# Optimization experiments

Hardware: AMD Instinct MI355X
Metric: run time of the kernel (lower is better)

The kernel has to match this reference:

```python
import jax, jax.numpy as jnp
import numpy as np

N_NODES = 50000
N_PAIRS = 200000
HID1 = 256
HID2 = 32


def gcn_conv(x, src, dst, W, b, n):
    # PyG GCNConv: project, add self-loops, sym-normalize, scatter-add to dst.
    sl = jnp.arange(n, dtype=src.dtype)
    s = jnp.concatenate([src, sl])
    d = jnp.concatenate([dst, sl])
    deg = jnp.zeros((n,), x.dtype).at[d].add(1.0)
    dinv = jax.lax.rsqrt(deg)  # deg >= 1 due to self-loops
    xw = x @ W  # [n, out]
    msg = xw[s] * (dinv[s] * dinv[d])[:, None]  # [E+n, out]
    out = jax.ops.segment_sum(msg, d, num_segments=n)
    return out + b


def setup_inputs() -> dict:
    key = jax.random.key(0)
    ks = jax.random.split(key, 16)
    inp = {
        "x": jax.random.randint(ks[0], (N_NODES,), 0, N_NODES),
        "edge1": jax.random.randint(ks[1], (2, 1600000), 0, N_NODES),
        "pos": jax.random.randint(ks[2], (N_PAIRS, 2), 0, N_NODES),
        "idx": jax.random.randint(ks[3], (N_PAIRS,), 0, N_PAIRS),
        "ei2": jax.random.randint(ks[4], (2, 1600000), 0, N_PAIRS),
        "emb_table": jax.random.normal(ks[5], (N_NODES + 1, HID1), jnp.float32) * 0.02,
        "W1": jax.random.normal(ks[6], (HID1, HID2), jnp.float32) * (1.0 / np.sqrt(HID1)),
        "b1": jnp.zeros((HID2,), jnp.float32),
        "W2a": jax.random.normal(ks[7], (HID2, HID2), jnp.float32) * (1.0 / np.sqrt(HID2)),
        "b2a": jnp.zeros((HID2,), jnp.float32),
        "W2b": jax.random.normal(ks[8], (HID2, HID2), jnp.float32) * (1.0 / np.sqrt(HID2)),
        "b2b": jnp.zeros((HID2,), jnp.float32),
        "Wp": jax.random.normal(ks[9], (HID2, 1), jnp.float32) * (1.0 / np.sqrt(HID2)),
        "bp": jnp.zeros((1,), jnp.float32),
    }
    return inp


def reference(x, edge1, pos, idx, ei2, emb_table, W1, b1, W2a, b2a, W2b, b2b, Wp, bp):
    # eval mode: all Dropouts are identity; no LayerNorm/GraphNorm (default flags False)
    h = emb_table[x]  # [N, HID1] embedding lookup (squeeze is no-op for 1D ids)
    # conv1s: single GCNConv HID1 -> HID2 + ReLU
    h = jax.nn.relu(gcn_conv(h, edge1[0], edge1[1], W1, b1, N_NODES))
    # pairwise gather-multiply over pos
    h = h[pos[:, 0]] * h[pos[:, 1]]  # [M, HID2]
    # conv2s / conv2s_r on the pair graph (edge2 = ei2, edge2_r = flipped)
    h = (jax.nn.relu(gcn_conv(h, ei2[0], ei2[1], W2a, b2a, N_PAIRS))
         + jax.nn.relu(gcn_conv(h, ei2[1], ei2[0], W2b, b2b, N_PAIRS)))
    # gather by idx, then multiply consecutive (even, odd) rows
    h = h[idx]  # [2Q, HID2]
    h = h[0::2] * h[1::2]  # [Q, HID2]
    return h @ Wp + bp  # [Q, 1]
```

## Files before the change

kernel.cpp:

```cpp
#include <hip/hip_runtime.h>
#include <hip/hip_fp16.h>
#include <math.h>


#define SL     256
#define SLOG   8
#define SL1    64
#define SLOG1  6
#define CAP    2432
#define SHIFT  18
#define BCH    8192
#define BT     1024
#define EPT    8
#define MAXSL2 1024
#define PB     64
#define EROW   264

typedef short bf16x8 __attribute__((ext_vector_type(8)));
typedef float f32x4 __attribute__((ext_vector_type(4)));

static __device__ __forceinline__ unsigned short f2bf(float f) {
    union { float f; unsigned u; } v;
    v.f = f;
    unsigned r = v.u + 0x7FFF + ((v.u >> 16) & 1);
    return (unsigned short)(r >> 16);
}
static __device__ __forceinline__ float bf2f(unsigned short h) {
    return __uint_as_float(((unsigned)h) << 16);
}
static __device__ __forceinline__ float bflo(unsigned u) { return __uint_as_float(u << 16); }
static __device__ __forceinline__ float bfhi(unsigned u) { return __uint_as_float(u & 0xFFFF0000u); }

static __device__ __forceinline__ float4 bfacc(float4 a, uint2 w) {
    a.x += bflo(w.x);
    a.y += bfhi(w.x);
    a.z += bflo(w.y);
    a.w += bfhi(w.y);
    return a;
}
static __device__ __forceinline__ float4 hacc(float4 a, uint2 w) {
    float2 f0 = __half22float2(*(__half2*)&w.x);
    float2 f1 = __half22float2(*(__half2*)&w.y);
    a.x += f0.x;
    a.y += f0.y;
    a.z += f1.x;
    a.w += f1.y;
    return a;
}
static __device__ __forceinline__ float4 h2f4(uint2 w) {
    float2 f0 = __half22float2(*(__half2*)&w.x);
    float2 f1 = __half22float2(*(__half2*)&w.y);
    float4 r = {f0.x, f0.y, f1.x, f1.y};
    return r;
}
static __device__ __forceinline__ uint2 f42h(float4 f) {
    __half2 h0 = __floats2half2_rn(f.x, f.y);
    __half2 h1 = __floats2half2_rn(f.z, f.w);
    uint2 r = {*(unsigned*)&h0, *(unsigned*)&h1};
    return r;
}

__global__ __launch_bounds__(256) void k_init(int* __restrict__ bumpF,
                                              int* __restrict__ bumpR,
                                              int* __restrict__ bump1,
                                              int NS2, int NS1) {
    int i = blockIdx.x * 256 + threadIdx.x;
    if (i < NS2) {
        bumpF[i] = i * CAP;
        bumpR[i] = i * CAP;
    }
    if (i < NS1) bump1[i] = i * CAP;
}

__global__ __launch_bounds__(BT) void k_build(const int* __restrict__ s2,
                                              const int* __restrict__ d2,
                                              const int* __restrict__ s1,
                                              const int* __restrict__ d1,
                                              int* bumpF, int* bumpR, int* bump1,
                                              int* __restrict__ bktF,
                                              int* __restrict__ bktR,
                                              int* __restrict__ bkt1,
                                              const float* __restrict__ W1,
                                              const float* __restrict__ W2a,
                                              const float* __restrict__ W2b,
                                              unsigned short* __restrict__ Wbhi,
                                              unsigned short* __restrict__ Wblo,
                                              unsigned short* __restrict__ W2ah,
                                              unsigned short* __restrict__ W2al,
                                              unsigned short* __restrict__ W2bh,
                                              unsigned short* __restrict__ W2bl,
                                              int E2, int E1, int NS2, int NS1,
                                              int NB2, int NB1) {
    __shared__ int stag[BCH];
    __shared__ unsigned short stag2[BCH];
    __shared__ int lbF[MAXSL2];
    __shared__ int lbR[MAXSL2];
    __shared__ int bgF[MAXSL2], bgR[MAXSL2];
    __shared__ int wsum[BT / 64];
    int tid = threadIdx.x, bid = blockIdx.x;
    int lane = tid & 63, wid = tid >> 6;

    auto exscan = [&](int v) -> int {
        int sc = v;
#pragma unroll
        for (int d = 1; d < 64; d <<= 1) {
            int t = __shfl_up(sc, d, 64);
            if (lane >= d) sc += t;
        }
        if (lane == 63) wsum[wid] = sc;
        __syncthreads();
        int woff = 0;
        for (int w2 = 0; w2 < wid; w2++) woff += wsum[w2];
        __syncthreads();
        return woff + sc - v;
    };

    if (bid < NB2) {
        if (tid < NS2) { lbF[tid] = 0; lbR[tid] = 0; }
        __syncthreads();
        int eb = bid * BCH;
        int n = E2 - eb; if (n > BCH) n = BCH;
        int sv[EPT], dv[EPT], ofF[EPT], ofR[EPT];
#pragma unroll
        for (int k = 0; k < EPT; k++) {
            int i = k * BT + tid;
            if (i < n) {
                sv[k] = s2[eb + i];
                dv[k] = d2[eb + i];
                ofF[k] = atomicAdd(&lbF[dv[k] >> SLOG], 1);
                ofR[k] = atomicAdd(&lbR[sv[k] >> SLOG], 1);
            }
        }
        __syncthreads();
        int cF = (tid < NS2) ? lbF[tid] : 0;
        int cR = (tid < NS2) ? lbR[tid] : 0;
        int preF = exscan(cF);
        int preR = exscan(cR);
        if (tid < NS2) {
            lbF[tid] = preF;
            lbR[tid] = preR;
            bgF[tid] = cF ? atomicAdd(&bumpF[tid], cF) : 0;
            bgR[tid] = cR ? atomicAdd(&bumpR[tid], cR) : 0;
        }
        __syncthreads();
#pragma unroll
        for (int k = 0; k < EPT; k++) {
            int i = k * BT + tid;
            if (i < n) {
                int sf = dv[k] >> SLOG;
                int p = lbF[sf] + ofF[k];
                stag[p] = ((dv[k] & (SL - 1)) << SHIFT) | sv[k];
                stag2[p] = (unsigned short)sf;
            }
        }
        __syncthreads();
        for (int i = tid; i < n; i += BT) {
            int sf = stag2[i];
            int gp = bgF[sf] + (i - lbF[sf]);
            if (gp < (sf + 1) * CAP) bktF[gp] = stag[i];
        }
        __syncthreads();
#pragma unroll
        for (int k = 0; k < EPT; k++) {
            int i = k * BT + tid;
            if (i < n) {
                int sr = sv[k] >> SLOG;
                int p = lbR[sr] + ofR[k];
                stag[p] = ((sv[k] & (SL - 1)) << SHIFT) | dv[k];
                stag2[p] = (unsigned short)sr;
            }
        }
        __syncthreads();
        for (int i = tid; i < n; i += BT) {
            int sr = stag2[i];
            int gp = bgR[sr] + (i - lbR[sr]);
            if (gp < (sr + 1) * CAP) bktR[gp] = stag[i];
        }
    } else if (bid < NB2 + NB1) {
        if (tid < NS1) lbF[tid] = 0;
        __syncthreads();
        int eb = (bid - NB2) * BCH;
        int n = E1 - eb; if (n > BCH) n = BCH;
        int sv[EPT], dv[EPT], of[EPT];
#pragma unroll
        for (int k = 0; k < EPT; k++) {
            int i = k * BT + tid;
            if (i < n) {
                sv[k] = s1[eb + i];
                dv[k] = d1[eb + i];
                of[k] = atomicAdd(&lbF[dv[k] >> SLOG1], 1);
            }
        }
        __syncthreads();
        int c = (tid < NS1) ? lbF[tid] : 0;
        int pre = exscan(c);
        if (tid < NS1) {
            lbF[tid] = pre;
            bgF[tid] = c ? atomicAdd(&bump1[tid], c) : 0;
        }
        __syncthreads();
#pragma unroll
        for (int k = 0; k < EPT; k++) {
            int i = k * BT + tid;
            if (i < n) {
                int sf = dv[k] >> SLOG1;
                int p = lbF[sf] + of[k];
                stag[p] = ((dv[k] & (SL1 - 1)) << SHIFT) | sv[k];
                stag2[p] = (unsigned short)sf;
            }
        }
        __syncthreads();
        for (int i = tid; i < n; i += BT) {
            int sf = stag2[i];
            int gp = bgF[sf] + (i - lbF[sf]);
            if (gp < (sf + 1) * CAP) bkt1[gp] = stag[i];
        }
    } else {
        int i = (bid - NB2 - NB1) * BT + tid;
        if (i < 8192) {
            int k = i >> 5, c = i & 31;
            float w = W1[i];
            unsigned short hi = f2bf(w);
            unsigned short lo = f2bf(w - bf2f(hi));
            Wbhi[c * 256 + k] = hi;
            Wblo[c * 256 + k] = lo;
        }
        if (i < 1024) {
            int k = i >> 5, c = i & 31;
            float wa = W2a[i], wb = W2b[i];
            unsigned short ha = f2bf(wa);
            unsigned short hb = f2bf(wb);
            W2ah[c * 32 + k] = ha;
            W2al[c * 32 + k] = f2bf(wa - bf2f(ha));
            W2bh[c * 32 + k] = hb;
            W2bl[c * 32 + k] = f2bf(wb - bf2f(hb));
        }
    }
}

__global__ __launch_bounds__(256) void k_sort(int* __restrict__ bkt1, const int* __restrict__ bump1,
                                              float* __restrict__ dinv1, int* __restrict__ beg1,
                                              int* __restrict__ cnt1,
                                              int* __restrict__ bktF, const int* __restrict__ bumpF,
                                              float* __restrict__ dinvF, int* __restrict__ begF,
                                              int* __restrict__ cntF,
                                              int* __restrict__ bktR, const int* __restrict__ bumpR,
                                              float* __restrict__ dinvR, int* __restrict__ begR,
                                              int* __restrict__ cntR,
                                              int NS1, int NS2, int N1, int NP) {
    __shared__ int sorted[CAP];
    __shared__ int hist[SL], cursor[SL];
    __shared__ int wsum[4];
    int bid = blockIdx.x, tid = threadIdx.x;
    int s, sls, N;
    int* bkt;
    const int* bump;
    float* dinv;
    int* beg;
    int* cntA;
    if (bid < NS1) {
        s = bid;
        bkt = bkt1; bump = bump1; dinv = dinv1; beg = beg1; cntA = cnt1;
        sls = SL1; N = N1;
    } else if (bid < NS1 + NS2) {
        s = bid - NS1;
        bkt = bktF; bump = bumpF; dinv = dinvF; beg = begF; cntA = cntF;
        sls = SL; N = NP;
    } else {
        s = bid - NS1 - NS2;
        bkt = bktR; bump = bumpR; dinv = dinvR; beg = begR; cntA = cntR;
        sls = SL; N = NP;
    }
    hist[tid] = 0;
    __syncthreads();
    int cnt = bump[s] - s * CAP;
    if (cnt > CAP) cnt = CAP;
    int* b = bkt + (size_t)s * CAP;
    for (int i = tid; i < cnt; i += 256) atomicAdd(&hist[b[i] >> SHIFT], 1);
    __syncthreads();
    int c = (tid < sls) ? hist[tid] : 0;
    int sc = c;
    int lane = tid & 63, wid = tid >> 6;
#pragma unroll
    for (int d = 1; d < 64; d <<= 1) {
        int t = __shfl_up(sc, d, 64);
        if (lane >= d) sc += t;
    }
    if (lane == 63) wsum[wid] = sc;
    __syncthreads();
    int woff = 0;
    for (int w = 0; w < wid; w++) woff += wsum[w];
    int pre = woff + sc - c;
    cursor[tid] = pre;
    if (tid < sls) {
        int v = s * sls + tid;
        if (v < N) {
            dinv[v] = 1.f / sqrtf((float)c + 1.f);
            beg[v] = s * CAP + pre;
            cntA[v] = c;
        }
    }
    __syncthreads();
    for (int i = tid; i < cnt; i += 256) {
        int pair = b[i];
        int dl = pair >> SHIFT;
        int p = atomicAdd(&cursor[dl], 1);
        sorted[p] = pair & ((1 << SHIFT) - 1);
    }
    __syncthreads();
    for (int i = tid; i < cnt; i += 256) b[i] = sorted[i];
}

__global__ __launch_bounds__(256) void k_xw1(const int* __restrict__ x,
                                             const float* __restrict__ emb,
                                             const unsigned short* __restrict__ Wbhi,
                                             const unsigned short* __restrict__ Wblo,
                                             const float* __restrict__ dinv1,
                                             __half* __restrict__ y1, int N) {
    __shared__ unsigned short sEhi[32 * EROW];
    __shared__ unsigned short sElo[32 * EROW];
    int tid = threadIdx.x;
    int lane = tid & 63, wv = tid >> 6;
    int r0 = blockIdx.x * 32;
    const float4* emb4 = (const float4*)emb;
#pragma unroll
    for (int p = 0; p < 8; p++) {
        int row = p * 4 + wv;
        int r = r0 + row;
        int xr = x[(r < N) ? r : 0];
        float4 e = emb4[(size_t)xr * 64 + lane];
        unsigned short h0 = f2bf(e.x), h1 = f2bf(e.y), h2 = f2bf(e.z), h3 = f2bf(e.w);
        ushort4 hi = {h0, h1, h2, h3};
        ushort4 lo = {f2bf(e.x - bf2f(h0)), f2bf(e.y - bf2f(h1)),
                      f2bf(e.z - bf2f(h2)), f2bf(e.w - bf2f(h3))};
        *(ushort4*)&sEhi[row * EROW + lane * 4] = hi;
        *(ushort4*)&sElo[row * EROW + lane * 4] = lo;
    }
    __syncthreads();
    int col = lane & 15, quad = lane >> 4;
    int rowtile = wv >> 1, ntile = wv & 1;
    f32x4 acc = {0.f, 0.f, 0.f, 0.f};
    const unsigned short* arow_hi = &sEhi[(rowtile * 16 + col) * EROW + quad * 8];
    const unsigned short* arow_lo = &sElo[(rowtile * 16 + col) * EROW + quad * 8];
    const unsigned short* bh = Wbhi + (ntile * 16 + col) * 256 + quad * 8;
    const unsigned short* bl = Wblo + (ntile * 16 + col) * 256 + quad * 8;
#pragma unroll
    for (int kb = 0; kb < 256; kb += 32) {
        bf16x8 ahi = *(const bf16x8*)(arow_hi + kb);
        bf16x8 alo = *(const bf16x8*)(arow_lo + kb);
        bf16x8 bhv = *(const bf16x8*)(bh + kb);
        bf16x8 blv = *(const bf16x8*)(bl + kb);
        acc = __builtin_amdgcn_mfma_f32_16x16x32_bf16(ahi, bhv, acc, 0, 0, 0);
        acc = __builtin_amdgcn_mfma_f32_16x16x32_bf16(alo, bhv, acc, 0, 0, 0);
        acc = __builtin_amdgcn_mfma_f32_16x16x32_bf16(ahi, blv, acc, 0, 0, 0);
    }
#pragma unroll
    for (int reg = 0; reg < 4; reg++) {
        int grow = r0 + rowtile * 16 + quad * 4 + reg;
        if (grow < N) {
            float dv = dinv1[grow];
            y1[grow * 32 + ntile * 16 + col] = __float2half(acc[reg] * dv);
        }
    }
}

static __device__ __forceinline__ float4 gcn_sum_h(const int* __restrict__ adj, int bg, int end,
                                                   const uint2* __restrict__ y2, int q,
                                                   float4 acc) {
    float4 a1 = {0.f, 0.f, 0.f, 0.f};
    int i = bg;
    for (; i + 4 <= end; i += 4) {
        int u0 = adj[i], u1 = adj[i + 1], u2 = adj[i + 2], u3 = adj[i + 3];
        uint2 w0 = y2[u0 * 8 + q];
        uint2 w1 = y2[u1 * 8 + q];
        uint2 w2 = y2[u2 * 8 + q];
        uint2 w3 = y2[u3 * 8 + q];
        acc = hacc(acc, w0);
        a1 = hacc(a1, w1);
        acc = hacc(acc, w2);
        a1 = hacc(a1, w3);
    }
    for (; i < end; i++) acc = hacc(acc, y2[adj[i] * 8 + q]);
    acc.x += a1.x;
    acc.y += a1.y;
    acc.z += a1.z;
    acc.w += a1.w;
    return acc;
}

static __device__ __forceinline__ float4 gcn_sum_bf(const int* __restrict__ adj, int bg, int end,
                                                    const uint2* __restrict__ y2, int q,
                                                    float4 acc) {
    float4 a1 = {0.f, 0.f, 0.f, 0.f};
    int i = bg;
    for (; i + 4 <= end; i += 4) {
        int u0 = adj[i], u1 = adj[i + 1], u2 = adj[i + 2], u3 = adj[i + 3];
        uint2 w0 = y2[u0 * 8 + q];
        uint2 w1 = y2[u1 * 8 + q];
        uint2 w2 = y2[u2 * 8 + q];
        uint2 w3 = y2[u3 * 8 + q];
        acc = bfacc(acc, w0);
        a1 = bfacc(a1, w1);
        acc = bfacc(acc, w2);
        a1 = bfacc(a1, w3);
    }
    for (; i < end; i++) acc = bfacc(acc, y2[adj[i] * 8 + q]);
    acc.x += a1.x;
    acc.y += a1.y;
    acc.z += a1.z;
    acc.w += a1.w;
    return acc;
}

__global__ __launch_bounds__(256) void k_gath1(const int* __restrict__ adj,
                                               const int* __restrict__ beg,
                                               const int* __restrict__ cntA,
                                               const float* __restrict__ dinv,
                                               const __half* __restrict__ y1,
                                               __half* __restrict__ out1, int N) {
    int gid = blockIdx.x * 256 + threadIdx.x;
    int v = gid >> 3, q = gid & 7;
    if (v >= N) return;
    int bg = beg[v];
    int end = bg + cntA[v];
    float dv = dinv[v];
    const uint2* y2 = (const uint2*)y1;
    float4 acc = {0.f, 0.f, 0.f, 0.f};
    acc = hacc(acc, y2[v * 8 + q]);
    acc = gcn_sum_h(adj, bg, end, y2, q, acc);
    acc.x *= dv;
    acc.y *= dv;
    acc.z *= dv;
    acc.w *= dv;
    ((uint2*)out1)[v * 8 + q] = f42h(acc);
}

__global__ __launch_bounds__(256) void k_gath2(const int* __restrict__ adjF,
                                               const int* __restrict__ begF,
                                               const int* __restrict__ cntF,
                                               const float* __restrict__ dinvF,
                                               const unsigned short* __restrict__ ya,
                                               const int* __restrict__ adjR,
                                               const int* __restrict__ begR,
                                               const int* __restrict__ cntR,
                                               const float* __restrict__ dinvR,
                                               const unsigned short* __restrict__ yb,
                                               const float* __restrict__ b2a,
                                               const float* __restrict__ b2b,
                                               __half* __restrict__ h3, int N) {
    int gid = blockIdx.x * 256 + threadIdx.x;
    int v = gid >> 3, q = gid & 7;
    if (v >= N) return;
    const uint2* ya2 = (const uint2*)ya;
    const uint2* yb2 = (const uint2*)yb;
    float4 aF = {0.f, 0.f, 0.f, 0.f};
    aF = bfacc(aF, ya2[v * 8 + q]);
    int bF = begF[v];
    aF = gcn_sum_bf(adjF, bF, bF + cntF[v], ya2, q, aF);
    float4 aR = {0.f, 0.f, 0.f, 0.f};
    aR = bfacc(aR, yb2[v * 8 + q]);
    int bR = begR[v];
    aR = gcn_sum_bf(adjR, bR, bR + cntR[v], yb2, q, aR);
    float dvF = dinvF[v], dvR = dinvR[v];
    float4 ba = ((const float4*)b2a)[q];
    float4 bb = ((const float4*)b2b)[q];
    float4 h;
    h.x = fmaxf(fmaf(aF.x, dvF, ba.x), 0.f) + fmaxf(fmaf(aR.x, dvR, bb.x), 0.f);
    h.y = fmaxf(fmaf(aF.y, dvF, ba.y), 0.f) + fmaxf(fmaf(aR.y, dvR, bb.y), 0.f);
    h.z = fmaxf(fmaf(aF.z, dvF, ba.z), 0.f) + fmaxf(fmaf(aR.z, dvR, bb.z), 0.f);
    h.w = fmaxf(fmaf(aF.w, dvF, ba.w), 0.f) + fmaxf(fmaf(aR.w, dvR, bb.w), 0.f);
    ((uint2*)h3)[v * 8 + q] = f42h(h);
}

__global__ __launch_bounds__(256) void k_xw2(const int* __restrict__ pos,
                                             const __half* __restrict__ out1,
                                             const float* __restrict__ b1,
                                             const unsigned short* __restrict__ W2ah,
                                             const unsigned short* __restrict__ W2al,
                                             const unsigned short* __restrict__ W2bh,
                                             const unsigned short* __restrict__ W2bl,
                                             const float* __restrict__ dinvF,
                                             const float* __restrict__ dinvR,
                                             unsigned short* __restrict__ ya,
                                             unsigned short* __restrict__ yb,
                                             int NP) {
    __shared__ unsigned short sHhi[PB * 32];
    __shared__ unsigned short sHlo[PB * 32];
    __shared__ int sPos[PB * 2];
    int tid = threadIdx.x;
    int p0 = blockIdx.x * PB;
    if (tid < PB * 2) {
        int gi = p0 * 2 + tid;
        sPos[tid] = (gi < NP * 2) ? pos[gi] : 0;
    }
    __syncthreads();
    const uint2* o12 = (const uint2*)out1;
    int q = tid & 7;
    float4 bq = ((const float4*)b1)[q];
#pragma unroll
    for (int half = 0; half < 2; half++) {
        int p = half * 32 + (tid >> 3);
        int ra = sPos[2 * p] * 8, rb = sPos[2 * p + 1] * 8;
        float4 ea = h2f4(o12[ra + q]);
        float4 eb = h2f4(o12[rb + q]);
        float4 h;
        h.x = fmaxf(ea.x + bq.x, 0.f) * fmaxf(eb.x + bq.x, 0.f);
        h.y = fmaxf(ea.y + bq.y, 0.f) * fmaxf(eb.y + bq.y, 0.f);
        h.z = fmaxf(ea.z + bq.z, 0.f) * fmaxf(eb.z + bq.z, 0.f);
        h.w = fmaxf(ea.w + bq.w, 0.f) * fmaxf(eb.w + bq.w, 0.f);
        unsigned short h0 = f2bf(h.x), h1 = f2bf(h.y), h2 = f2bf(h.z), h3 = f2bf(h.w);
        ushort4 hi = {h0, h1, h2, h3};
        ushort4 lo = {f2bf(h.x - bf2f(h0)), f2bf(h.y - bf2f(h1)),
                      f2bf(h.z - bf2f(h2)), f2bf(h.w - bf2f(h3))};
        *(ushort4*)&sHhi[p * 32 + q * 4] = hi;
        *(ushort4*)&sHlo[p * 32 + q * 4] = lo;
    }
    __syncthreads();
    int lane = tid & 63, wv = tid >> 6;
    int col = lane & 15, quad = lane >> 4;
    bf16x8 ahi = *(const bf16x8*)&sHhi[(wv * 16 + col) * 32 + quad * 8];
    bf16x8 alo = *(const bf16x8*)&sHlo[(wv * 16 + col) * 32 + quad * 8];
    f32x4 accA[2], accB[2];
#pragma unroll
    for (int nt = 0; nt < 2; nt++) {
        int off = (nt * 16 + col) * 32 + quad * 8;
        bf16x8 bah = *(const bf16x8*)(W2ah + off);
        bf16x8 bal = *(const bf16x8*)(W2al + off);
        bf16x8 bbh = *(const bf16x8*)(W2bh + off);
        bf16x8 bbl = *(const bf16x8*)(W2bl + off);
        f32x4 z = {0.f, 0.f, 0.f, 0.f};
        f32x4 a = __builtin_amdgcn_mfma_f32_16x16x32_bf16(ahi, bah, z, 0, 0, 0);
        a = __builtin_amdgcn_mfma_f32_16x16x32_bf16(alo, bah, a, 0, 0, 0);
        a = __builtin_amdgcn_mfma_f32_16x16x32_bf16(ahi, bal, a, 0, 0, 0);
        accA[nt] = a;
        f32x4 b = __builtin_amdgcn_mfma_f32_16x16x32_bf16(ahi, bbh, z, 0, 0, 0);
        b = __builtin_amdgcn_mfma_f32_16x16x32_bf16(alo, bbh, b, 0, 0, 0);
        b = __builtin_amdgcn_mfma_f32_16x16x32_bf16(ahi, bbl, b, 0, 0, 0);
        accB[nt] = b;
    }
#pragma unroll
    for (int reg = 0; reg < 4; reg++) {
        int p = wv * 16 + quad * 4 + reg;
        int pg = p0 + p;
        if (pg < NP) {
            float dA = dinvF[pg], dB = dinvR[pg];
#pragma unroll
            for (int nt = 0; nt < 2; nt++) {
                ya[pg * 32 + nt * 16 + col] = f2bf(accA[nt][reg] * dA);
                yb[pg * 32 + nt * 16 + col] = f2bf(accB[nt][reg] * dB);
            }
        }
    }
}

__global__ __launch_bounds__(256) void k_final(const int* __restrict__ idx,
                                               const __half* __restrict__ h3,
                                               const float* __restrict__ Wp,
                                               const float* __restrict__ bp,
                                               float* __restrict__ out, int Q) {
    int gid = blockIdx.x * 256 + threadIdx.x;
    int qi = gid >> 3, q = gid & 7;
    if (qi >= Q) return;
    int i0 = idx[2 * qi] * 8, i1 = idx[2 * qi + 1] * 8;
    float4 wp = ((const float4*)Wp)[q];
    const uint2* H = (const uint2*)h3;
    float4 h0 = h2f4(H[i0 + q]), h1 = h2f4(H[i1 + q]);
    float s = h0.x * h1.x * wp.x + h0.y * h1.y * wp.y + h0.z * h1.z * wp.z + h0.w * h1.w * wp.w;
    s += __shfl_xor(s, 1);
    s += __shfl_xor(s, 2);
    s += __shfl_xor(s, 4);
    if (q == 0) out[qi] = s + bp[0];
}

extern "C" void kernel_launch(void* const* d_in, const int* in_sizes, int n_in,
                              void* d_out, int out_size, void* d_ws, size_t ws_size,
                              hipStream_t stream) {
    const int* x    = (const int*)d_in[0];
    const int* e1   = (const int*)d_in[1];
    const int* pos  = (const int*)d_in[2];
    const int* idx  = (const int*)d_in[3];
    const int* e2   = (const int*)d_in[4];
    const float* emb = (const float*)d_in[5];
    const float* W1  = (const float*)d_in[6];
    const float* b1  = (const float*)d_in[7];
    const float* W2a = (const float*)d_in[8];
    const float* b2a = (const float*)d_in[9];
    const float* W2b = (const float*)d_in[10];
    const float* b2b = (const float*)d_in[11];
    const float* Wp  = (const float*)d_in[12];
    const float* bp  = (const float*)d_in[13];

    const int N1 = in_sizes[0];
    const int E1 = in_sizes[1] / 2;
    const int NP = in_sizes[3];
    const int E2 = in_sizes[4] / 2;
    const int Q  = out_size;
    (void)n_in; (void)ws_size;

    const int NS1 = (N1 + SL1 - 1) >> SLOG1;
    const int NS2 = (NP + SL - 1) >> SLOG;

    char* w = (char*)d_ws;
    size_t o = 0;
    auto alloc = [&](size_t bytes) { size_t r = o; o += (bytes + 255) & ~(size_t)255; return r; };
    float* dinv1  = (float*)(w + alloc((size_t)(N1 + 2 * NP) * 4));
    float* dinv2f = dinv1 + N1;
    float* dinv2r = dinv2f + NP;
    int* beg1  = (int*)(w + alloc((size_t)(N1 + 2 * NP) * 4));
    int* beg2f = beg1 + N1;
    int* beg2r = beg2f + NP;
    int* cnt1  = (int*)(w + alloc((size_t)(N1 + 2 * NP) * 4));
    int* cnt2f = cnt1 + N1;
    int* cnt2r = cnt2f + NP;
    int* bumpF = (int*)(w + alloc((size_t)(2 * NS2 + NS1) * 4));
    int* bumpR = bumpF + NS2;
    int* bump1 = bumpR + NS2;
    unsigned short* Wbhi = (unsigned short*)(w + alloc(8192 * 2));
    unsigned short* Wblo = (unsigned short*)(w + alloc(8192 * 2));
    unsigned short* W2ah = (unsigned short*)(w + alloc(1024 * 2));
    unsigned short* W2al = (unsigned short*)(w + alloc(1024 * 2));
    unsigned short* W2bh = (unsigned short*)(w + alloc(1024 * 2));
    unsigned short* W2bl = (unsigned short*)(w + alloc(1024 * 2));
    int* bktF = (int*)(w + alloc((size_t)NS2 * CAP * 4));
    int* bktR = (int*)(w + alloc((size_t)NS2 * CAP * 4));
    int* bkt1 = (int*)(w + alloc((size_t)NS1 * CAP * 4));
    __half* out1 = (__half*)(w + alloc((size_t)N1 * 32 * 2));
    __half* y1   = (__half*)(w + alloc((size_t)N1 * 32 * 2));
    unsigned short* ya = (unsigned short*)(w + alloc((size_t)NP * 32 * 2));
    unsigned short* yb = (unsigned short*)(w + alloc((size_t)NP * 32 * 2));
    __half* h3  = (__half*)(w + alloc((size_t)NP * 32 * 2));

    const int B = 256;
    auto cdiv = [](long long a, long long b) { return (int)((a + b - 1) / b); };
    const int NB2 = cdiv(E2, BCH), NB1 = cdiv(E1, BCH);
    const int NBW = cdiv(8192, BT);

    k_init<<<cdiv(NS2 > NS1 ? NS2 : NS1, B), B, 0, stream>>>(bumpF, bumpR, bump1, NS2, NS1);
    k_build<<<NB2 + NB1 + NBW, BT, 0, stream>>>(e2, e2 + E2, e1, e1 + E1,
                                                bumpF, bumpR, bump1, bktF, bktR, bkt1,
                                                W1, W2a, W2b, Wbhi, Wblo,
                                                W2ah, W2al, W2bh, W2bl,
                                                E2, E1, NS2, NS1, NB2, NB1);
    k_sort<<<NS1 + 2 * NS2, B, 0, stream>>>(bkt1, bump1, dinv1, beg1, cnt1,
                                            bktF, bumpF, dinv2f, beg2f, cnt2f,
                                            bktR, bumpR, dinv2r, beg2r, cnt2r,
                                            NS1, NS2, N1, NP);
    k_xw1<<<cdiv(N1, 32), B, 0, stream>>>(x, emb, Wbhi, Wblo, dinv1, y1, N1);
    k_gath1<<<cdiv((long long)N1 * 8, B), B, 0, stream>>>(bkt1, beg1, cnt1, dinv1, y1, out1, N1);
    k_xw2<<<cdiv(NP, PB), B, 0, stream>>>(pos, out1, b1, W2ah, W2al, W2bh, W2bl,
                                          dinv2f, dinv2r, ya, yb, NP);
    k_gath2<<<cdiv((long long)NP * 8, B), B, 0, stream>>>(bktF, beg2f, cnt2f, dinv2f, ya,
                                                          bktR, beg2r, cnt2r, dinv2r, yb,
                                                          b2a, b2b, h3, NP);
    k_final<<<cdiv((long long)Q * 8, B), B, 0, stream>>>(idx, h3, Wp, bp, (float*)d_out, Q);
}
```

Before: 281.0 us.

## Presort bucket edges by source range before dst sort; unroll layer-1 gather by 8

The per-bucket counting sort becomes a two-pass radix sort. Edges are first grouped by coarse source-node range (src>>10) and then stably by destination, so each destination's neighbour list comes out ordered by source index. This aims to improve locality of the feature gathers in the aggregation kernels. The layer-1 gather loop also gets an 8-wide unrolled path for more loads in flight. The cost is an extra shared-memory array, extra atomics and two more scan barriers in the sort kernel.

```diff
diff --git a/kernel.cpp b/kernel.cpp
--- a/kernel.cpp
+++ b/kernel.cpp
@@ -9,6 +9,7 @@
 #define SLOG1  6
 #define CAP    2432
 #define SHIFT  18
+#define NMASK  ((1 << SHIFT) - 1)
 #define BCH    8192
 #define BT     1024
 #define EPT    8
@@ -248,8 +249,9 @@
                                               float* __restrict__ dinvR, int* __restrict__ begR,
                                               int* __restrict__ cntR,
                                               int NS1, int NS2, int N1, int NP) {
-    __shared__ int sorted[CAP];
-    __shared__ int hist[SL], cursor[SL];
+    __shared__ int A[CAP];
+    __shared__ int S[CAP];
+    __shared__ int hN[SL], hD[SL];
     __shared__ int wsum[4];
     int bid = blockIdx.x, tid = threadIdx.x;
     int s, sls, N;
@@ -271,44 +273,61 @@
         bkt = bktR; bump = bumpR; dinv = dinvR; beg = begR; cntA = cntR;
         sls = SL; N = NP;
     }
-    hist[tid] = 0;
+    hN[tid] = 0;
+    hD[tid] = 0;
     __syncthreads();
     int cnt = bump[s] - s * CAP;
     if (cnt > CAP) cnt = CAP;
     int* b = bkt + (size_t)s * CAP;
-    for (int i = tid; i < cnt; i += 256) atomicAdd(&hist[b[i] >> SHIFT], 1);
-    __syncthreads();
-    int c = (tid < sls) ? hist[tid] : 0;
-    int sc = c;
+    for (int i = tid; i < cnt; i += 256) {
+        int e = b[i];
+        atomicAdd(&hN[(e & NMASK) >> 10], 1);
+        atomicAdd(&hD[e >> SHIFT], 1);
+    }
+    __syncthreads();
+    int cn = hN[tid];
+    int cd = hD[tid];
     int lane = tid & 63, wid = tid >> 6;
-#pragma unroll
-    for (int d = 1; d < 64; d <<= 1) {
-        int t = __shfl_up(sc, d, 64);
-        if (lane >= d) sc += t;
-    }
-    if (lane == 63) wsum[wid] = sc;
-    __syncthreads();
-    int woff = 0;
-    for (int w = 0; w < wid; w++) woff += wsum[w];
-    int pre = woff + sc - c;
-    cursor[tid] = pre;
+    auto exscan = [&](int v) -> int {
+        int sc = v;
+#pragma unroll
+        for (int d = 1; d < 64; d <<= 1) {
+            int t = __shfl_up(sc, d, 64);
+            if (lane >= d) sc += t;
+        }
+        if (lane == 63) wsum[wid] = sc;
+        __syncthreads();
+        int woff = 0;
+        for (int w = 0; w < wid; w++) woff += wsum[w];
+        __syncthreads();
+        return woff + sc - v;
+    };
+    int preN = exscan(cn);
+    int preD = exscan(cd);
+    hN[tid] = preN;
+    hD[tid] = preD;
     if (tid < sls) {
         int v = s * sls + tid;
         if (v < N) {
-            dinv[v] = 1.f / sqrtf((float)c + 1.f);
-            beg[v] = s * CAP + pre;
-            cntA[v] = c;
+            dinv[v] = 1.f / sqrtf((float)cd + 1.f);
+            beg[v] = s * CAP + preD;
+            cntA[v] = cd;
         }
     }
     __syncthreads();
     for (int i = tid; i < cnt; i += 256) {
-        int pair = b[i];
-        int dl = pair >> SHIFT;
-        int p = atomicAdd(&cursor[dl], 1);
-        sorted[p] = pair & ((1 << SHIFT) - 1);
-    }
-    __syncthreads();
-    for (int i = tid; i < cnt; i += 256) b[i] = sorted[i];
+        int e = b[i];
+        int p = atomicAdd(&hN[(e & NMASK) >> 10], 1);
+        A[p] = e;
+    }
+    __syncthreads();
+    for (int i = tid; i < cnt; i += 256) {
+        int e = A[i];
+        int p = atomicAdd(&hD[e >> SHIFT], 1);
+        S[p] = e & NMASK;
+    }
+    __syncthreads();
+    for (int i = tid; i < cnt; i += 256) b[i] = S[i];
 }
 
 __global__ __launch_bounds__(256) void k_xw1(const int* __restrict__ x,
@@ -364,11 +383,31 @@
     }
 }
 
-static __device__ __forceinline__ float4 gcn_sum_h(const int* __restrict__ adj, int bg, int end,
-                                                   const uint2* __restrict__ y2, int q,
-                                                   float4 acc) {
+static __device__ __forceinline__ float4 gcn_sum_h8(const int* __restrict__ adj, int bg, int end,
+                                                    const uint2* __restrict__ y2, int q,
+                                                    float4 acc) {
     float4 a1 = {0.f, 0.f, 0.f, 0.f};
     int i = bg;
+    for (; i + 8 <= end; i += 8) {
+        int u0 = adj[i], u1 = adj[i + 1], u2 = adj[i + 2], u3 = adj[i + 3];
+        int u4 = adj[i + 4], u5 = adj[i + 5], u6 = adj[i + 6], u7 = adj[i + 7];
+        uint2 w0 = y2[u0 * 8 + q];
+        uint2 w1 = y2[u1 * 8 + q];
+        uint2 w2 = y2[u2 * 8 + q];
+        uint2 w3 = y2[u3 * 8 + q];
+        uint2 w4 = y2[u4 * 8 + q];
+        uint2 w5 = y2[u5 * 8 + q];
+        uint2 w6 = y2[u6 * 8 + q];
+        uint2 w7 = y2[u7 * 8 + q];
+        acc = hacc(acc, w0);
+        a1 = hacc(a1, w1);
+        acc = hacc(acc, w2);
+        a1 = hacc(a1, w3);
+        acc = hacc(acc, w4);
+        a1 = hacc(a1, w5);
+        acc = hacc(acc, w6);
+        a1 = hacc(a1, w7);
+    }
     for (; i + 4 <= end; i += 4) {
         int u0 = adj[i], u1 = adj[i + 1], u2 = adj[i + 2], u3 = adj[i + 3];
         uint2 w0 = y2[u0 * 8 + q];
@@ -427,7 +466,7 @@
     const uint2* y2 = (const uint2*)y1;
     float4 acc = {0.f, 0.f, 0.f, 0.f};
     acc = hacc(acc, y2[v * 8 + q]);
-    acc = gcn_sum_h(adj, bg, end, y2, q, acc);
+    acc = gcn_sum_h8(adj, bg, end, y2, q, acc);
     acc.x *= dv;
     acc.y *= dv;
     acc.z *= dv;
```

After: 280.0 us. About the same (-0.3%).
